# Kernel tuning notes

Measured on AMD Instinct MI355X. Metric: run time of the kernel, lower is better.

## Reference

```python
import jax, jax.numpy as jnp
import numpy as np

B = 4096          # batch
F = 1024          # feature_count * embedding_dim
E = 16            # embedding_dim (domain embedding)
D = 8             # num_domains
T = F + E         # cross-net total dim
L = 3             # cross layers
EPS = 1e-5


def setup_inputs() -> dict:
    key = jax.random.key(0)
    ks = jax.random.split(key, 32)
    s = 0.02
    inp = {}
    inp["x"] = jax.random.normal(ks[0], (B, F), dtype=jnp.float32)
    inp["domain_ids"] = jax.random.randint(ks[1], (B,), 0, D)
    # partitioned normalization params
    inp["pn_weight"] = jnp.ones((D, F), jnp.float32)
    inp["pn_bias"] = jnp.zeros((D, F), jnp.float32)
    # domain embedding table
    inp["dom_emb"] = jax.random.normal(ks[2], (D, E), jnp.float32) * 0.1
    # cross network: L layers, each Linear(T->1, no bias) + additive bias vector
    inp["cross_w"] = jax.random.normal(ks[3], (L, T), jnp.float32) * s
    inp["cross_b"] = jnp.zeros((L, T), jnp.float32)
    # center MLP: T->512->256->128 (ReLU, ReLU, none)
    inp["cW1"] = jax.random.normal(ks[4], (T, 512), jnp.float32) * s
    inp["cb1"] = jnp.zeros((512,), jnp.float32)
    inp["cW2"] = jax.random.normal(ks[5], (512, 256), jnp.float32) * s
    inp["cb2"] = jnp.zeros((256,), jnp.float32)
    inp["cW3"] = jax.random.normal(ks[6], (256, 128), jnp.float32) * s
    inp["cb3"] = jnp.zeros((128,), jnp.float32)
    # per-domain nets: T->512->256->128; last bias initialized to domain_net_init_bias=1.0
    inp["dW1"] = jax.random.normal(ks[7], (D, T, 512), jnp.float32) * s
    inp["db1"] = jnp.zeros((D, 512), jnp.float32)
    inp["dW2"] = jax.random.normal(ks[8], (D, 512, 256), jnp.float32) * s
    inp["db2"] = jnp.zeros((D, 256), jnp.float32)
    inp["dW3"] = jax.random.normal(ks[9], (D, 256, 128), jnp.float32) * s
    inp["db3"] = jnp.ones((D, 128), jnp.float32)
    # final MLP: 128->64->1
    inp["fW1"] = jax.random.normal(ks[10], (128, 64), jnp.float32) * s
    inp["fb1"] = jnp.zeros((64,), jnp.float32)
    inp["fW2"] = jax.random.normal(ks[11], (64, 1), jnp.float32) * s
    inp["fb2"] = jnp.zeros((1,), jnp.float32)
    # auxiliary net: E->32->1
    inp["aW1"] = jax.random.normal(ks[12], (E, 32), jnp.float32) * s
    inp["ab1"] = jnp.zeros((32,), jnp.float32)
    inp["aW2"] = jax.random.normal(ks[13], (32, 1), jnp.float32) * s
    inp["ab2"] = jnp.zeros((1,), jnp.float32)
    return inp


def _forward(x, domain_ids, pn_weight, pn_bias, dom_emb, cross_w, cross_b,
             cW1, cb1, cW2, cb2, cW3, cb3,
             dW1, db1, dW2, db2, dW3, db3,
             fW1, fb1, fW2, fb2, aW1, ab1, aW2, ab2):
    # --- PartitionedNormalization: per-sample LayerNorm stats + domain-indexed affine ---
    mean = jnp.mean(x, axis=1, keepdims=True)
    var = jnp.mean((x - mean) ** 2, axis=1, keepdims=True)  # unbiased=False
    normed = (x - mean) / jnp.sqrt(var + EPS)
    normed = normed * pn_weight[domain_ids] + pn_bias[domain_ids]

    xd = dom_emb[domain_ids]                    # (B, E)
    x0 = jnp.concatenate([normed, xd], axis=1)  # (B, T)

    # --- CrossNetworkWithDomain ---
    xc = x0
    for i in range(L):
        proj = xc @ cross_w[i]                  # (B,)
        xc = x0 * proj[:, None] + cross_b[i] + xc

    # --- center MLP ---
    h = jax.nn.relu(xc @ cW1 + cb1)
    h = jax.nn.relu(h @ cW2 + cb2)
    h_center = h @ cW3 + cb3                    # (B, 128)

    # --- domain-specific nets: run all D nets, select per-sample ---
    a = jax.nn.relu(jnp.einsum('bi,dio->bdo', xc, dW1) + db1[None])   # (B, D, 512)
    a = jax.nn.relu(jnp.einsum('bdi,dio->bdo', a, dW2) + db2[None])   # (B, D, 256)
    a = jnp.einsum('bdi,dio->bdo', a, dW3) + db3[None]                # (B, D, 128)
    h_domain = a[jnp.arange(a.shape[0]), domain_ids]                  # (B, 128)

    # --- STAR fusion (tanh) ---
    fused = h_center * jnp.tanh(h_domain)

    # --- final MLP + auxiliary net ---
    main_logits = jax.nn.relu(fused @ fW1 + fb1) @ fW2 + fb2          # (B, 1)
    aux_logits = jax.nn.relu(xd @ aW1 + ab1) @ aW2 + ab2              # (B, 1)
    return jax.nn.sigmoid(main_logits + aux_logits)


def reference(x, domain_ids, pn_weight, pn_bias, dom_emb, cross_w, cross_b,
              cW1, cb1, cW2, cb2, cW3, cb3,
              dW1, db1, dW2, db2, dW3, db3,
              fW1, fb1, fW2, fb2, aW1, ab1, aW2, ab2):
    return _forward(x, domain_ids, pn_weight, pn_bias, dom_emb, cross_w, cross_b,
                    cW1, cb1, cW2, cb2, cW3, cb3,
                    dW1, db1, dW2, db2, dW3, db3,
                    fW1, fb1, fW2, fb2, aW1, ab1, aW2, ab2)
```

## Files before the change

kernel.cpp:

```cpp
#include <hip/hip_runtime.h>
#include <math.h>
#include <stdint.h>

#define BATCH 4096
#define FEAT  1024
#define EDIM  16
#define NDOM  8
#define TDIM  1040
#define KP1   1088
#define NLAYER 3
#define EPSV  1e-5f

typedef __attribute__((ext_vector_type(8))) short bf16x8;
typedef __attribute__((ext_vector_type(4))) float f32x4;

__device__ __forceinline__ unsigned short f2bf(float f) {
    union { float f; unsigned int u; } v; v.f = f;
    unsigned int u = v.u;
    return (unsigned short)((u + 0x7fffu + ((u >> 16) & 1u)) >> 16);
}
__device__ __forceinline__ float bf2f(unsigned short u) {
    union { unsigned int u; float f; } v; v.u = ((unsigned int)u) << 16; return v.f;
}
__device__ __forceinline__ void gload_lds16(const void* g, void* l) {
    __builtin_amdgcn_global_load_lds(
        (const __attribute__((address_space(1))) void*)(g),
        (__attribute__((address_space(3))) void*)(l), 16, 0, 0);
}

#define T_W1 136
#define T_W2 32
#define T_W3 8
#define NCONV (T_W1*9 + T_W2*9 + T_W3*9)

__global__ __launch_bounds__(256) void front(
    const int* __restrict__ dom, int* __restrict__ perm, int* __restrict__ starts,
    const float* __restrict__ cW1, const float* __restrict__ dW1,
    const float* __restrict__ cW2, const float* __restrict__ dW2,
    const float* __restrict__ cW3, const float* __restrict__ dW3,
    unsigned short* __restrict__ Wc1b, unsigned short* __restrict__ Wd1b,
    unsigned short* __restrict__ Wc2b, unsigned short* __restrict__ Wd2b,
    unsigned short* __restrict__ Wc3b, unsigned short* __restrict__ Wd3b,
    const float* __restrict__ x,
    const float* __restrict__ pnw, const float* __restrict__ pnb,
    const float* __restrict__ demb,
    const float* __restrict__ crw, const float* __restrict__ crb,
    const float* __restrict__ aW1, const float* __restrict__ ab1,
    const float* __restrict__ aW2, const float* __restrict__ ab2,
    unsigned short* __restrict__ XCb, float* __restrict__ auxg) {
    int b = blockIdx.x;
    int t = threadIdx.x;

    if (b < NCONV) {
        __shared__ float tile[64][65];
        const float* src; unsigned short* dst; int K, N, Kp, rr;
        if (b < T_W1)            { src = cW1; dst = Wc1b; K = TDIM; N = 512; Kp = KP1; rr = b; }
        else if (b < T_W1*9)     { int r = b - T_W1; int z = r / T_W1; rr = r % T_W1;
                                   src = dW1 + (size_t)z * TDIM * 512; dst = Wd1b + (size_t)z * 512 * KP1;
                                   K = TDIM; N = 512; Kp = KP1; }
        else if (b < T_W1*9+T_W2)   { src = cW2; dst = Wc2b; K = 512; N = 256; Kp = 512; rr = b - T_W1*9; }
        else if (b < T_W1*9+T_W2*9) { int r = b - (T_W1*9+T_W2); int z = r / T_W2; rr = r % T_W2;
                                   src = dW2 + (size_t)z * 512 * 256; dst = Wd2b + (size_t)z * 256 * 512;
                                   K = 512; N = 256; Kp = 512; }
        else if (b < T_W1*9+T_W2*9+T_W3) { src = cW3; dst = Wc3b; K = 256; N = 128; Kp = 256; rr = b - (T_W1*9+T_W2*9); }
        else                     { int r = b - (T_W1*9+T_W2*9+T_W3); int z = r / T_W3; rr = r % T_W3;
                                   src = dW3 + (size_t)z * 256 * 128; dst = Wd3b + (size_t)z * 128 * 256;
                                   K = 256; N = 128; Kp = 256; }
        int kt = Kp >> 6;
        int kb = rr % kt, nb = rr / kt;
        int k0 = kb * 64, n0 = nb * 64;
        #pragma unroll
        for (int i = 0; i < 4; i++) {
            int flat = t + i * 256;
            int kr = flat >> 4, c4 = flat & 15;
            int k = k0 + kr;
            float4 v = make_float4(0.f, 0.f, 0.f, 0.f);
            if (k < K) v = *(const float4*)(src + (size_t)k * N + n0 + c4 * 4);
            tile[kr][c4 * 4 + 0] = v.x;
            tile[kr][c4 * 4 + 1] = v.y;
            tile[kr][c4 * 4 + 2] = v.z;
            tile[kr][c4 * 4 + 3] = v.w;
        }
        __syncthreads();
        #pragma unroll
        for (int i = 0; i < 4; i++) {
            int flat = t + i * 256;
            int n = flat >> 4, kg = flat & 15;
            ushort4 sv;
            sv.x = f2bf(tile[kg * 4 + 0][n]);
            sv.y = f2bf(tile[kg * 4 + 1][n]);
            sv.z = f2bf(tile[kg * 4 + 2][n]);
            sv.w = f2bf(tile[kg * 4 + 3][n]);
            *(ushort4*)(dst + (size_t)(n0 + n) * Kp + k0 + kg * 4) = sv;
        }
        return;
    }
    if (b == NCONV) {
        __shared__ int cnt[NDOM];
        __shared__ int off[NDOM];
        if (t < NDOM) cnt[t] = 0;
        __syncthreads();
        for (int i = t; i < BATCH; i += 256) atomicAdd(&cnt[dom[i]], 1);
        __syncthreads();
        if (t == 0) {
            int s = 0;
            for (int d = 0; d < NDOM; d++) { off[d] = s; starts[d] = s; s += cnt[d]; }
            starts[NDOM] = s;
        }
        __syncthreads();
        for (int i = t; i < BATCH; i += 256) {
            int p = atomicAdd(&off[dom[i]], 1);
            perm[p] = i;
        }
        return;
    }

    int w = t >> 6, lane = t & 63;
    int row = (b - NCONV - 1) * 4 + w;
    int d = dom[row];

    float4 X[4];
    #pragma unroll
    for (int j = 0; j < 4; j++)
        X[j] = *(const float4*)(x + (size_t)row * FEAT + 4 * lane + 256 * j);

    float s = 0.f, ss = 0.f;
    #pragma unroll
    for (int j = 0; j < 4; j++) {
        s  += X[j].x + X[j].y + X[j].z + X[j].w;
        ss += X[j].x*X[j].x + X[j].y*X[j].y + X[j].z*X[j].z + X[j].w*X[j].w;
    }
    #pragma unroll
    for (int m = 1; m < 64; m <<= 1) {
        s  += __shfl_xor(s,  m);
        ss += __shfl_xor(ss, m);
    }
    float mean = s / (float)FEAT;
    float var  = ss / (float)FEAT - mean * mean;
    float rstd = rsqrtf(var + EPSV);

    float4 x0[4], xc[4];
    #pragma unroll
    for (int j = 0; j < 4; j++) {
        float4 wv = *(const float4*)(pnw + (size_t)d * FEAT + 4 * lane + 256 * j);
        float4 bv = *(const float4*)(pnb + (size_t)d * FEAT + 4 * lane + 256 * j);
        x0[j].x = (X[j].x - mean) * rstd * wv.x + bv.x;
        x0[j].y = (X[j].y - mean) * rstd * wv.y + bv.y;
        x0[j].z = (X[j].z - mean) * rstd * wv.z + bv.z;
        x0[j].w = (X[j].w - mean) * rstd * wv.w + bv.w;
        xc[j] = x0[j];
    }
    float x0e = 0.f, xce = 0.f;
    if (lane < EDIM) { x0e = demb[d * EDIM + lane]; xce = x0e; }

    #pragma unroll
    for (int l = 0; l < NLAYER; l++) {
        const float* wl = crw + l * TDIM;
        const float* bl = crb + l * TDIM;
        float partial = 0.f;
        #pragma unroll
        for (int j = 0; j < 4; j++) {
            float4 wv = *(const float4*)(wl + 4 * lane + 256 * j);
            partial += xc[j].x*wv.x + xc[j].y*wv.y + xc[j].z*wv.z + xc[j].w*wv.w;
        }
        if (lane < EDIM) partial += xce * wl[FEAT + lane];
        #pragma unroll
        for (int m = 1; m < 64; m <<= 1) partial += __shfl_xor(partial, m);
        float proj = partial;
        #pragma unroll
        for (int j = 0; j < 4; j++) {
            float4 bv = *(const float4*)(bl + 4 * lane + 256 * j);
            xc[j].x = fmaf(x0[j].x, proj, bv.x + xc[j].x);
            xc[j].y = fmaf(x0[j].y, proj, bv.y + xc[j].y);
            xc[j].z = fmaf(x0[j].z, proj, bv.z + xc[j].z);
            xc[j].w = fmaf(x0[j].w, proj, bv.w + xc[j].w);
        }
        if (lane < EDIM) xce = fmaf(x0e, proj, bl[FEAT + lane] + xce);
    }

    #pragma unroll
    for (int j = 0; j < 4; j++) {
        ushort4 sv;
        sv.x = f2bf(xc[j].x); sv.y = f2bf(xc[j].y);
        sv.z = f2bf(xc[j].z); sv.w = f2bf(xc[j].w);
        *(ushort4*)(XCb + (size_t)row * KP1 + 4 * lane + 256 * j) = sv;
    }
    XCb[(size_t)row * KP1 + FEAT + lane] = (lane < EDIM) ? f2bf(xce) : 0;

    float h = (lane < 32) ? ab1[lane] : 0.f;
    #pragma unroll
    for (int e = 0; e < EDIM; e++) {
        float ev = __shfl(xce, e);
        if (lane < 32) h = fmaf(ev, aW1[e * 32 + lane], h);
    }
    float c = (lane < 32) ? fmaxf(h, 0.f) * aW2[lane] : 0.f;
    #pragma unroll
    for (int m = 1; m < 64; m <<= 1) c += __shfl_xor(c, m);
    if (lane == 0) auxg[row] = c + ab2[0];
}

__global__ __launch_bounds__(256) void gemm_l1_fused(
    const unsigned short* __restrict__ A,
    const unsigned short* __restrict__ Wc,
    const unsigned short* __restrict__ Wd,
    const float* __restrict__ bc, const float* __restrict__ bd,
    unsigned short* __restrict__ Cc, unsigned short* __restrict__ Cd,
    const int* __restrict__ starts, const int* __restrict__ perm) {
    __shared__ short As[128 * 64];
    __shared__ short Bs[128 * 64];

    int y = blockIdx.y;
    int d = y >> 5, sl = y & 31;
    int ds = starts[d], de = starts[d + 1];
    int m0 = ds + sl * 128;
    if (m0 >= de) return;
    int mEnd = de;
    int n0 = blockIdx.x * 64;

    int tid = threadIdx.x;
    int w = tid >> 6, lane = tid & 63;
    int wm = w >> 1, wn = w & 1;
    int lr = lane & 15, q = lane >> 4;

    const unsigned short* pA[4]; short* dA[4];
    const unsigned short* pB[4]; short* dB[4];
    #pragma unroll
    for (int i = 0; i < 4; i++) {
        int seg = i * 4 + w;
        int ch = seg * 64 + lane;
        int loc = ch >> 3, c = ch & 7;
        int mm = m0 + loc; if (mm > mEnd - 1) mm = mEnd - 1;
        int rowp = perm[mm];
        pA[i] = A + (size_t)rowp * KP1 + ((c ^ (loc & 7)) << 3);
        dA[i] = As + seg * 512;
    }
    #pragma unroll
    for (int i = 0; i < 4; i++) {
        int seg = i * 4 + w;
        int ch = seg * 64 + lane;
        int loc = ch >> 3, c = ch & 7;
        const unsigned short* base = (loc < 64)
            ? (Wc + (size_t)(n0 + loc) * KP1)
            : (Wd + ((size_t)d * 512 + n0 + (loc - 64)) * KP1);
        pB[i] = base + ((c ^ (loc & 7)) << 3);
        dB[i] = Bs + seg * 512;
    }

    f32x4 acc[4][4];
    #pragma unroll
    for (int i = 0; i < 4; i++)
        #pragma unroll
        for (int j = 0; j < 4; j++)
            acc[i][j] = (f32x4){0.f, 0.f, 0.f, 0.f};

    for (int k0 = 0; k0 < KP1; k0 += 64) {
        #pragma unroll
        for (int i = 0; i < 4; i++) gload_lds16(pA[i] + k0, dA[i]);
        #pragma unroll
        for (int i = 0; i < 4; i++) gload_lds16(pB[i] + k0, dB[i]);
        __syncthreads();

        #pragma unroll
        for (int half = 0; half < 2; half++) {
            int cc = half * 4 + q;
            bf16x8 af[4], bf[4];
            #pragma unroll
            for (int i = 0; i < 4; i++) {
                int m = wm * 64 + i * 16 + lr;
                af[i] = *(const bf16x8*)(As + m * 64 + ((cc ^ (m & 7)) << 3));
            }
            #pragma unroll
            for (int j = 0; j < 4; j++) {
                int n = wn * 64 + j * 16 + lr;
                bf[j] = *(const bf16x8*)(Bs + n * 64 + ((cc ^ (n & 7)) << 3));
            }
            #pragma unroll
            for (int i = 0; i < 4; i++)
                #pragma unroll
                for (int j = 0; j < 4; j++)
                    acc[i][j] = __builtin_amdgcn_mfma_f32_16x16x32_bf16(
                        af[i], bf[j], acc[i][j], 0, 0, 0);
        }
        __syncthreads();
    }

    const float* bias = wn ? (bd + d * 512) : bc;
    unsigned short* C = wn ? Cd : Cc;
    #pragma unroll
    for (int i = 0; i < 4; i++) {
        #pragma unroll
        for (int j = 0; j < 4; j++) {
            int col = n0 + j * 16 + lr;
            float bvv = bias[col];
            int rowb = m0 + wm * 64 + i * 16 + q * 4;
            #pragma unroll
            for (int r = 0; r < 4; r++) {
                int row = rowb + r;
                if (row >= mEnd) continue;
                C[(size_t)row * 512 + col] = f2bf(fmaxf(acc[i][j][r] + bvv, 0.f));
            }
        }
    }
}

__global__ __launch_bounds__(256) void tail_fused(
    const unsigned short* __restrict__ H1c, const unsigned short* __restrict__ H1d,
    const unsigned short* __restrict__ Wc2, const unsigned short* __restrict__ Wd2,
    const float* __restrict__ cb2v, const float* __restrict__ db2v,
    const unsigned short* __restrict__ Wc3, const unsigned short* __restrict__ Wd3,
    const float* __restrict__ cb3v, const float* __restrict__ db3v,
    const float* __restrict__ fW1, const float* __restrict__ fb1,
    const float* __restrict__ fW2, const float* __restrict__ fb2,
    const float* __restrict__ auxg, const int* __restrict__ perm,
    const int* __restrict__ starts, float* __restrict__ out) {

    __shared__ __align__(16) char smem[98304];
    short* Bsb[2] = { (short*)smem, (short*)(smem + 32768) };
    short* Asb[2] = { (short*)(smem + 65536), (short*)(smem + 69632) };
    short* H2    = (short*)(smem + 73728);
    short* fused = (short*)(smem + 90112);

    int y = blockIdx.x;
    int d = y >> 7, sl = y & 127;
    int ds = starts[d], de = starts[d + 1];
    int m0 = ds + sl * 32;
    if (m0 >= de) return;
    int mEnd = de;

    int tid = threadIdx.x;
    int w = tid >> 6, lane = tid & 63;
    int lr = lane & 15, q = lane >> 4;

    int bn = w * 8 + (lane >> 3);
    int sw = ((lane & 7) ^ (bn & 7)) << 3;
    int rowA = m0 + bn; if (rowA > mEnd - 1) rowA = mEnd - 1;

    const unsigned short* pA0  = H1c + (size_t)rowA * 512 + sw;
    const unsigned short* pA1  = H1d + (size_t)rowA * 512 + sw;
    const unsigned short* pW20 = Wc2 + (size_t)bn * 512 + sw;
    const unsigned short* pW21 = Wd2 + (size_t)d * 256 * 512 + (size_t)bn * 512 + sw;
    const unsigned short* pW30 = Wc3 + (size_t)bn * 256 + sw;
    const unsigned short* pW31 = Wd3 + (size_t)d * 128 * 256 + (size_t)bn * 256 + sw;

    auto stage_l2 = [&](int c, int k0, int pb) {
        const unsigned short* pa = c ? pA1 : pA0;
        const unsigned short* pw = c ? pW21 : pW20;
        gload_lds16(pa + k0, Asb[pb] + w * 512);
        #pragma unroll
        for (int i = 0; i < 8; i++)
            gload_lds16(pw + (size_t)i * 32 * 512 + k0, Bsb[pb] + (i * 4 + w) * 512);
    };
    auto stage_l3 = [&](int c, int k0, int pb) {
        const unsigned short* pw = c ? pW31 : pW30;
        #pragma unroll
        for (int i = 0; i < 4; i++)
            gload_lds16(pw + (size_t)i * 32 * 256 + k0, Bsb[pb] + (i * 4 + w) * 512);
    };

    stage_l2(0, 0, 0);
    __syncthreads();

    #pragma unroll
    for (int c = 0; c < 2; c++) {
        f32x4 acc2[2][4];
        #pragma unroll
        for (int i = 0; i < 2; i++)
            #pragma unroll
            for (int j = 0; j < 4; j++) acc2[i][j] = (f32x4){0.f, 0.f, 0.f, 0.f};

        #pragma unroll
        for (int it = 0; it < 8; it++) {
            int t = c * 12 + it;
            int pb = t & 1, pn = pb ^ 1;
            if (it < 7) stage_l2(c, (it + 1) * 64, pn);
            else        stage_l3(c, 0, pn);

            #pragma unroll
            for (int half = 0; half < 2; half++) {
                int cc = half * 4 + q;
                bf16x8 af[2], bf[4];
                #pragma unroll
                for (int i = 0; i < 2; i++) {
                    int m = i * 16 + lr;
                    af[i] = *(const bf16x8*)(Asb[pb] + m * 64 + ((cc ^ (m & 7)) << 3));
                }
                #pragma unroll
                for (int j = 0; j < 4; j++) {
                    int n = w * 64 + j * 16 + lr;
                    bf[j] = *(const bf16x8*)(Bsb[pb] + n * 64 + ((cc ^ (n & 7)) << 3));
                }
                #pragma unroll
                for (int i = 0; i < 2; i++)
                    #pragma unroll
                    for (int j = 0; j < 4; j++)
                        acc2[i][j] = __builtin_amdgcn_mfma_f32_16x16x32_bf16(
                            af[i], bf[j], acc2[i][j], 0, 0, 0);
            }
            __syncthreads();
        }

        const float* b2 = c ? (db2v + d * 256) : cb2v;
        #pragma unroll
        for (int i = 0; i < 2; i++)
            #pragma unroll
            for (int j = 0; j < 4; j++) {
                int col = w * 64 + j * 16 + lr;
                float bv = b2[col];
                int cch = col >> 3;
                #pragma unroll
                for (int r = 0; r < 4; r++) {
                    int row = i * 16 + q * 4 + r;
                    int pc = (cch & 24) | ((cch ^ (row & 7)) & 7);
                    float v = fmaxf(acc2[i][j][r] + bv, 0.f);
                    H2[row * 256 + pc * 8 + (col & 7)] = (short)f2bf(v);
                }
            }
        __syncthreads();

        f32x4 acc3[2][2];
        #pragma unroll
        for (int i = 0; i < 2; i++)
            #pragma unroll
            for (int j = 0; j < 2; j++) acc3[i][j] = (f32x4){0.f, 0.f, 0.f, 0.f};

        #pragma unroll
        for (int it = 0; it < 4; it++) {
            int t = c * 12 + 8 + it;
            int pb = t & 1, pn = pb ^ 1;
            if (it < 3)      stage_l3(c, (it + 1) * 64, pn);
            else if (c == 0) stage_l2(1, 0, pn);

            #pragma unroll
            for (int half = 0; half < 2; half++) {
                int cc = half * 4 + q;
                int C = it * 8 + cc;
                bf16x8 af[2], bf[2];
                #pragma unroll
                for (int i = 0; i < 2; i++) {
                    int m = i * 16 + lr;
                    int pcm = (C & 24) | ((C ^ (m & 7)) & 7);
                    af[i] = *(const bf16x8*)(H2 + m * 256 + pcm * 8);
                }
                #pragma unroll
                for (int j = 0; j < 2; j++) {
                    int n = w * 32 + j * 16 + lr;
                    bf[j] = *(const bf16x8*)(Bsb[pb] + n * 64 + ((cc ^ (n & 7)) << 3));
                }
                #pragma unroll
                for (int i = 0; i < 2; i++)
                    #pragma unroll
                    for (int j = 0; j < 2; j++)
                        acc3[i][j] = __builtin_amdgcn_mfma_f32_16x16x32_bf16(
                            af[i], bf[j], acc3[i][j], 0, 0, 0);
            }
            __syncthreads();
        }

        const float* b3 = c ? (db3v + d * 128) : cb3v;
        #pragma unroll
        for (int i = 0; i < 2; i++)
            #pragma unroll
            for (int j = 0; j < 2; j++) {
                int col = w * 32 + j * 16 + lr;
                float bv = b3[col];
                int cch = col >> 3;
                #pragma unroll
                for (int r = 0; r < 4; r++) {
                    int row = i * 16 + q * 4 + r;
                    int pc = (cch & 8) | ((cch ^ (row & 7)) & 7);
                    int idx = row * 128 + pc * 8 + (col & 7);
                    if (c == 0) {
                        fused[idx] = (short)f2bf(acc3[i][j][r] + bv);
                    } else {
                        float cv = bf2f((unsigned short)fused[idx]);
                        fused[idx] = (short)f2bf(cv * tanhf(acc3[i][j][r] + bv));
                    }
                }
            }
        __syncthreads();
    }

    short* Bsf = Bsb[0];
    float* Ls  = (float*)Asb[0];
    for (int s2 = tid; s2 < 1024; s2 += 256) {
        int n = s2 >> 4, cch = s2 & 15;
        bf16x8 vv;
        #pragma unroll
        for (int kk = 0; kk < 8; kk++)
            vv[kk] = (short)f2bf(fW1[(cch * 8 + kk) * 64 + n]);
        int pc = (cch & 8) | ((cch ^ (n & 7)) & 7);
        *(bf16x8*)(Bsf + n * 128 + pc * 8) = vv;
    }
    __syncthreads();

    int wm = w >> 1, wn = w & 1;
    f32x4 acc2f[2];
    #pragma unroll
    for (int j = 0; j < 2; j++) acc2f[j] = (f32x4){0.f, 0.f, 0.f, 0.f};
    #pragma unroll
    for (int g = 0; g < 4; g++) {
        int cc = g * 4 + q;
        int m = wm * 16 + lr;
        int pcm = (cc & 8) | ((cc ^ (m & 7)) & 7);
        bf16x8 af = *(const bf16x8*)(fused + m * 128 + pcm * 8);
        #pragma unroll
        for (int j = 0; j < 2; j++) {
            int n = wn * 32 + j * 16 + lr;
            int pcn = (cc & 8) | ((cc ^ (n & 7)) & 7);
            bf16x8 bf = *(const bf16x8*)(Bsf + n * 128 + pcn * 8);
            acc2f[j] = __builtin_amdgcn_mfma_f32_16x16x32_bf16(af, bf, acc2f[j], 0, 0, 0);
        }
    }

    float w2v[2], b1v[2];
    #pragma unroll
    for (int j = 0; j < 2; j++) {
        int col = wn * 32 + j * 16 + lr;
        w2v[j] = fW2[col];
        b1v[j] = fb1[col];
    }
    float rowv[4];
    #pragma unroll
    for (int r = 0; r < 4; r++) {
        float v = 0.f;
        #pragma unroll
        for (int j = 0; j < 2; j++)
            v += fmaxf(acc2f[j][r] + b1v[j], 0.f) * w2v[j];
        v += __shfl_xor(v, 1);
        v += __shfl_xor(v, 2);
        v += __shfl_xor(v, 4);
        v += __shfl_xor(v, 8);
        rowv[r] = v;
    }
    if (wn == 0 && lr == 0) {
        #pragma unroll
        for (int r = 0; r < 4; r++)
            Ls[wm * 16 + q * 4 + r] = rowv[r];
    }
    __syncthreads();
    if (wn == 1 && lr == 0) {
        float b2 = fb2[0];
        #pragma unroll
        for (int r = 0; r < 4; r++) {
            int row = wm * 16 + q * 4 + r;
            int p = m0 + row;
            if (p < mEnd) {
                int orow = perm[p];
                float logit = Ls[row] + rowv[r] + b2 + auxg[orow];
                out[orow] = 1.f / (1.f + expf(-logit));
            }
        }
    }
}

extern "C" void kernel_launch(void* const* d_in, const int* in_sizes, int n_in,
                              void* d_out, int out_size, void* d_ws, size_t ws_size,
                              hipStream_t stream) {
    (void)in_sizes; (void)n_in; (void)out_size; (void)ws_size;

    const float* x    = (const float*)d_in[0];
    const int*   dom  = (const int*)  d_in[1];
    const float* pnw  = (const float*)d_in[2];
    const float* pnb  = (const float*)d_in[3];
    const float* demb = (const float*)d_in[4];
    const float* crw  = (const float*)d_in[5];
    const float* crb  = (const float*)d_in[6];
    const float* cW1  = (const float*)d_in[7];
    const float* cb1  = (const float*)d_in[8];
    const float* cW2  = (const float*)d_in[9];
    const float* cb2  = (const float*)d_in[10];
    const float* cW3  = (const float*)d_in[11];
    const float* cb3  = (const float*)d_in[12];
    const float* dW1  = (const float*)d_in[13];
    const float* db1  = (const float*)d_in[14];
    const float* dW2  = (const float*)d_in[15];
    const float* db2  = (const float*)d_in[16];
    const float* dW3  = (const float*)d_in[17];
    const float* db3  = (const float*)d_in[18];
    const float* fW1  = (const float*)d_in[19];
    const float* fb1  = (const float*)d_in[20];
    const float* fW2  = (const float*)d_in[21];
    const float* fb2  = (const float*)d_in[22];
    const float* aW1  = (const float*)d_in[23];
    const float* ab1  = (const float*)d_in[24];
    const float* aW2  = (const float*)d_in[25];
    const float* ab2  = (const float*)d_in[26];
    float* out = (float*)d_out;

    char* base = (char*)d_ws;
    size_t o = 0;
    auto alloc = [&](size_t bytes) { char* p = base + o; o += (bytes + 255) & ~size_t(255); return p; };

    int* perm   = (int*)alloc(BATCH * 4);
    int* starts = (int*)alloc((NDOM + 1) * 4);
    float* auxg = (float*)alloc(BATCH * 4);
    unsigned short* XCb  = (unsigned short*)alloc((size_t)BATCH * KP1 * 2);
    unsigned short* H1c  = (unsigned short*)alloc((size_t)BATCH * 512 * 2);
    unsigned short* H1d  = (unsigned short*)alloc((size_t)BATCH * 512 * 2);
    unsigned short* Wc1b = (unsigned short*)alloc((size_t)512 * KP1 * 2);
    unsigned short* Wd1b = (unsigned short*)alloc((size_t)NDOM * 512 * KP1 * 2);
    unsigned short* Wc2b = (unsigned short*)alloc((size_t)256 * 512 * 2);
    unsigned short* Wd2b = (unsigned short*)alloc((size_t)NDOM * 256 * 512 * 2);
    unsigned short* Wc3b = (unsigned short*)alloc((size_t)128 * 256 * 2);
    unsigned short* Wd3b = (unsigned short*)alloc((size_t)NDOM * 128 * 256 * 2);

    front<<<NCONV + 1 + BATCH / 4, 256, 0, stream>>>(
        dom, perm, starts, cW1, dW1, cW2, dW2, cW3, dW3,
        Wc1b, Wd1b, Wc2b, Wd2b, Wc3b, Wd3b,
        x, pnw, pnb, demb, crw, crb, aW1, ab1, aW2, ab2, XCb, auxg);

    gemm_l1_fused<<<dim3(512 / 64, NDOM * 32), 256, 0, stream>>>(
        XCb, Wc1b, Wd1b, cb1, db1, H1c, H1d, starts, perm);

    tail_fused<<<NDOM * 128, 256, 0, stream>>>(
        H1c, H1d, Wc2b, Wd2b, cb2, db2, Wc3b, Wd3b, cb3, db3,
        fW1, fb1, fW2, fb2, auxg, perm, starts, out);
}
```

Baseline: 191.8 us.

## Double-buffer LDS in layer-1 GEMM and reorder block grids across domains

The layer-1 GEMM now keeps two LDS buffers for A and B. It issues the global-to-LDS loads for the next K step before the MFMAs on the current step, so there is one barrier per iteration. The goal is to hide global load latency behind matrix math. The cost is twice the LDS per block (64 KB), which may lower occupancy. The GEMM grid is transposed so domain/row slices vary fastest, and the tail kernel interleaves domains in its block index. Both spread early-exiting empty blocks more evenly and change how weights are reused in cache.

```diff
diff --git a/kernel.cpp b/kernel.cpp
--- a/kernel.cpp
+++ b/kernel.cpp
@@ -206,24 +206,24 @@
     const float* __restrict__ bc, const float* __restrict__ bd,
     unsigned short* __restrict__ Cc, unsigned short* __restrict__ Cd,
     const int* __restrict__ starts, const int* __restrict__ perm) {
-    __shared__ short As[128 * 64];
-    __shared__ short Bs[128 * 64];
-
-    int y = blockIdx.y;
-    int d = y >> 5, sl = y & 31;
+    __shared__ short As[2][128 * 64];
+    __shared__ short Bs[2][128 * 64];
+
+    int xb = blockIdx.x;
+    int d = xb >> 5, sl = xb & 31;
     int ds = starts[d], de = starts[d + 1];
     int m0 = ds + sl * 128;
     if (m0 >= de) return;
     int mEnd = de;
-    int n0 = blockIdx.x * 64;
+    int n0 = blockIdx.y * 64;
 
     int tid = threadIdx.x;
     int w = tid >> 6, lane = tid & 63;
     int wm = w >> 1, wn = w & 1;
     int lr = lane & 15, q = lane >> 4;
 
-    const unsigned short* pA[4]; short* dA[4];
-    const unsigned short* pB[4]; short* dB[4];
+    const unsigned short* pA[4]; int sA[4];
+    const unsigned short* pB[4]; int sB[4];
     #pragma unroll
     for (int i = 0; i < 4; i++) {
         int seg = i * 4 + w;
@@ -232,7 +232,7 @@
         int mm = m0 + loc; if (mm > mEnd - 1) mm = mEnd - 1;
         int rowp = perm[mm];
         pA[i] = A + (size_t)rowp * KP1 + ((c ^ (loc & 7)) << 3);
-        dA[i] = As + seg * 512;
+        sA[i] = seg * 512;
     }
     #pragma unroll
     for (int i = 0; i < 4; i++) {
@@ -243,7 +243,7 @@
             ? (Wc + (size_t)(n0 + loc) * KP1)
             : (Wd + ((size_t)d * 512 + n0 + (loc - 64)) * KP1);
         pB[i] = base + ((c ^ (loc & 7)) << 3);
-        dB[i] = Bs + seg * 512;
+        sB[i] = seg * 512;
     }
 
     f32x4 acc[4][4];
@@ -253,13 +253,22 @@
         for (int j = 0; j < 4; j++)
             acc[i][j] = (f32x4){0.f, 0.f, 0.f, 0.f};
 
-    for (int k0 = 0; k0 < KP1; k0 += 64) {
-        #pragma unroll
-        for (int i = 0; i < 4; i++) gload_lds16(pA[i] + k0, dA[i]);
-        #pragma unroll
-        for (int i = 0; i < 4; i++) gload_lds16(pB[i] + k0, dB[i]);
-        __syncthreads();
-
+    #pragma unroll
+    for (int i = 0; i < 4; i++) gload_lds16(pA[i], As[0] + sA[i]);
+    #pragma unroll
+    for (int i = 0; i < 4; i++) gload_lds16(pB[i], Bs[0] + sB[i]);
+    __syncthreads();
+
+    #pragma unroll 1
+    for (int ks = 0; ks < KP1 / 64; ks++) {
+        int cur = ks & 1, nxt = cur ^ 1;
+        if (ks < KP1 / 64 - 1) {
+            int k0 = (ks + 1) * 64;
+            #pragma unroll
+            for (int i = 0; i < 4; i++) gload_lds16(pA[i] + k0, As[nxt] + sA[i]);
+            #pragma unroll
+            for (int i = 0; i < 4; i++) gload_lds16(pB[i] + k0, Bs[nxt] + sB[i]);
+        }
         #pragma unroll
         for (int half = 0; half < 2; half++) {
             int cc = half * 4 + q;
@@ -267,12 +276,12 @@
             #pragma unroll
             for (int i = 0; i < 4; i++) {
                 int m = wm * 64 + i * 16 + lr;
-                af[i] = *(const bf16x8*)(As + m * 64 + ((cc ^ (m & 7)) << 3));
+                af[i] = *(const bf16x8*)(As[cur] + m * 64 + ((cc ^ (m & 7)) << 3));
             }
             #pragma unroll
             for (int j = 0; j < 4; j++) {
                 int n = wn * 64 + j * 16 + lr;
-                bf[j] = *(const bf16x8*)(Bs + n * 64 + ((cc ^ (n & 7)) << 3));
+                bf[j] = *(const bf16x8*)(Bs[cur] + n * 64 + ((cc ^ (n & 7)) << 3));
             }
             #pragma unroll
             for (int i = 0; i < 4; i++)
@@ -321,7 +330,7 @@
     short* fused = (short*)(smem + 90112);
 
     int y = blockIdx.x;
-    int d = y >> 7, sl = y & 127;
+    int d = y & 7, sl = y >> 3;
     int ds = starts[d], de = starts[d + 1];
     int m0 = ds + sl * 32;
     if (m0 >= de) return;
@@ -609,7 +618,7 @@
         Wc1b, Wd1b, Wc2b, Wd2b, Wc3b, Wd3b,
         x, pnw, pnb, demb, crw, crb, aW1, ab1, aW2, ab2, XCb, auxg);
 
-    gemm_l1_fused<<<dim3(512 / 64, NDOM * 32), 256, 0, stream>>>(
+    gemm_l1_fused<<<dim3(NDOM * 32, 8), 256, 0, stream>>>(
         XCb, Wc1b, Wd1b, cb1, db1, H1c, H1d, starts, perm);
 
     tail_fused<<<NDOM * 128, 256, 0, stream>>>(
```

Measured after the change: 260.9 us. +36.0%, slower.
